# Performance work log

Hardware: AMD Instinct MI355X
Metric: run time of the kernel (lower is better)

The kernel has to match this reference:

```python
import jax, jax.numpy as jnp
import numpy as np

K = 16      # neighbors per node (hard-coded in ParticleNet)
EPS = 1e-5  # BatchNorm eps


def _forward(x, convs, fcW1, fcb1, fcW2, fcb2):
    # x: [B, N, F0]; convs: list of 3 layer-lists of (W, b, gamma, beta)
    B, N, _ = x.shape
    for c, layers in enumerate(convs):
        feat = x[..., :2] if c == 0 else x            # first kNN uses coords only
        sq = jnp.sum(feat * feat, axis=-1)            # [B, N]
        d2 = sq[:, :, None] + sq[:, None, :] - 2.0 * jnp.einsum('bnf,bmf->bnm', feat, feat)
        d2 = d2 + jnp.eye(N, dtype=d2.dtype) * 1e9    # exclude self-loops (knn_graph loop=False)
        idx = jax.lax.top_k(-d2, K)[1]                # [B, N, K] nearest-neighbor indices
        x_j = jax.vmap(lambda xb, ib: xb[ib])(x, idx) # gather neighbors -> [B, N, K, F]
        x_i = jnp.broadcast_to(x[:, :, None, :], x_j.shape)
        h = jnp.concatenate([x_i, x_j - x_i], axis=-1)  # PyG EdgeConv message input
        for (W, b, g, e) in layers:                   # Linear -> BatchNorm1d(train) -> ReLU
            h = h @ W + b
            m = h.mean(axis=(0, 1, 2))
            v = h.var(axis=(0, 1, 2))
            h = jax.nn.relu(g * (h - m) * jax.lax.rsqrt(v + EPS) + e)
        x = jnp.concatenate([h.mean(axis=2), x], axis=-1)  # aggr='mean', then skip-concat
    pooled = x.mean(axis=1)                           # global_mean_pool -> [B, 451]
    return (pooled @ fcW1 + fcb1) @ fcW2 + fcb2       # fc1 (no act) then fc2


def setup_inputs() -> dict:
    key = jax.random.key(0)
    B, N, F = 128, 128, 3
    ins, outs = [6, 134, 390], [64, 128, 256]
    d = {}
    ki = [0]
    def nk():
        ki[0] += 1
        return jax.random.fold_in(key, ki[0])
    d['x'] = jax.random.normal(nk(), (B, N, F), jnp.float32)
    for c in range(3):
        dims = [(ins[c], outs[c]), (outs[c], outs[c]), (outs[c], outs[c])]
        for l, (fi, fo) in enumerate(dims):
            d[f'W{c}{l}'] = jax.random.normal(nk(), (fi, fo), jnp.float32) / np.sqrt(fi).astype(np.float32)
            d[f'b{c}{l}'] = jnp.zeros((fo,), jnp.float32)
            d[f'g{c}{l}'] = jnp.ones((fo,), jnp.float32)
            d[f'e{c}{l}'] = jnp.zeros((fo,), jnp.float32)
    d['fcW1'] = jax.random.normal(nk(), (451, 256), jnp.float32) / np.float32(np.sqrt(451))
    d['fcb1'] = jnp.zeros((256,), jnp.float32)
    d['fcW2'] = jax.random.normal(nk(), (256, 5), jnp.float32) / np.float32(np.sqrt(256))
    d['fcb2'] = jnp.zeros((5,), jnp.float32)
    return d


def reference(x,
              W00, b00, g00, e00, W01, b01, g01, e01, W02, b02, g02, e02,
              W10, b10, g10, e10, W11, b11, g11, e11, W12, b12, g12, e12,
              W20, b20, g20, e20, W21, b21, g21, e21, W22, b22, g22, e22,
              fcW1, fcb1, fcW2, fcb2):
    convs = [
        [(W00, b00, g00, e00), (W01, b01, g01, e01), (W02, b02, g02, e02)],
        [(W10, b10, g10, e10), (W11, b11, g11, e11), (W12, b12, g12, e12)],
        [(W20, b20, g20, e20), (W21, b21, g21, e21), (W22, b22, g22, e22)],
    ]
    return _forward(x, convs, fcW1, fcb1, fcW2, fcb2)
```

## Files before the change

kernel.cpp:

```cpp
#include <hip/hip_runtime.h>
#include <hip/hip_bf16.h>
#include <type_traits>

typedef __hip_bfloat16 bf16;
typedef short v8s __attribute__((ext_vector_type(8)));
typedef short v2s __attribute__((ext_vector_type(2)));
typedef float v4f __attribute__((ext_vector_type(4)));

__device__ __forceinline__ float b2f(bf16 v) { return __bfloat162float(v); }
__device__ __forceinline__ bf16  f2b(float v) { return __float2bfloat16(v); }
__device__ __forceinline__ short f2bs(float v) {
    bf16 b = f2b(v); short s; __builtin_memcpy(&s, &b, 2); return s;
}
__device__ __forceinline__ float bs2f(short s) {
    bf16 b; __builtin_memcpy(&b, &s, 2); return b2f(b);
}

#define NB 128
#define NN 128
#define KNN 16
#define M_NODES (NB * NN)
#define NPOS ((long)M_NODES * KNN)
#define NREP 16

__device__ __forceinline__ void fold_stats(const float* __restrict__ st, int c,
                                           float& sum, float& sq) {
    sum = 0.f; sq = 0.f;
#pragma unroll
    for (int r = 0; r < NREP; ++r) { sum += st[r * 512 + c]; sq += st[r * 512 + 256 + c]; }
}

__device__ __forceinline__ int swz_tile(int bid) {
    int xcd = bid & 7;
    int slot = bid >> 3;
    int batch = xcd * 16 + (slot >> 5);
    int tile = slot & 31;
    return batch * 32 + tile;
}

__global__ void zero_kernel(float* __restrict__ p, int n) {
    int i = blockIdx.x * blockDim.x + threadIdx.x;
    if (i < n) p[i] = 0.f;
}

__global__ __launch_bounds__(256) void wconv_kernel(const float* __restrict__ W,
        short* __restrict__ Wt, int O) {
    int d = blockIdx.x * 256 + threadIdx.x;
    int c = d / O, k = d - c * O;
    Wt[d] = f2bs(W[(size_t)k * O + c]);
}

__global__ __launch_bounds__(256) void wconv0_kernel(const float* __restrict__ W,
        short* __restrict__ Wd, short* __restrict__ Wb, int F, int Fpad, int O) {
    int d = blockIdx.x * 256 + threadIdx.x;
    if (d >= O * Fpad) return;
    int c = d / Fpad, k = d - c * Fpad;
    if (k < F) {
        float wt = W[(size_t)k * O + c];
        float wb = W[(size_t)(F + k) * O + c];
        Wd[d] = f2bs(wt - wb);
        Wb[d] = f2bs(wb);
    } else { Wd[d] = 0; Wb[d] = 0; }
}

__global__ __launch_bounds__(256) void sq_kernel(const float* __restrict__ x, int C, int D,
                                                 float* __restrict__ sq) {
    int n = blockIdx.x * 256 + threadIdx.x;
    if (n >= M_NODES) return;
    float s = 0.f;
    for (int d = 0; d < D; ++d) { float v = x[(size_t)n * C + d]; s += v * v; }
    sq[n] = s;
}

__global__ __launch_bounds__(256) void dist_kernel(const float* __restrict__ x, int C, int D,
                                                   const float* __restrict__ sq,
                                                   float* __restrict__ d2) {
    __shared__ float As[16][65];
    __shared__ float Bs[16][65];
    const int tid = threadIdx.x;
    const int tx = tid & 15, ty = tid >> 4;
    const int m0 = blockIdx.y * 64;
    const int b  = m0 >> 7;
    const int c0 = blockIdx.x * 64;
    float acc[4][4];
#pragma unroll
    for (int r = 0; r < 4; ++r)
#pragma unroll
        for (int c = 0; c < 4; ++c) acc[r][c] = 0.f;
    for (int k0 = 0; k0 < D; k0 += 16) {
        for (int l = tid; l < 1024; l += 256) {
            int k = l & 15, m = l >> 4;
            int kk = k0 + k;
            As[k][m] = (kk < D) ? x[(size_t)(m0 + m) * C + kk] : 0.f;
            Bs[k][m] = (kk < D) ? x[(size_t)(b * NN + c0 + m) * C + kk] : 0.f;
        }
        __syncthreads();
        for (int k = 0; k < 16; ++k) {
            float av[4], bv[4];
#pragma unroll
            for (int r = 0; r < 4; ++r) av[r] = As[k][ty + 16 * r];
#pragma unroll
            for (int c = 0; c < 4; ++c) bv[c] = Bs[k][tx + 16 * c];
#pragma unroll
            for (int r = 0; r < 4; ++r)
#pragma unroll
                for (int c = 0; c < 4; ++c) acc[r][c] += av[r] * bv[c];
        }
        __syncthreads();
    }
#pragma unroll
    for (int r = 0; r < 4; ++r)
#pragma unroll
        for (int c = 0; c < 4; ++c) {
            int m = m0 + ty + 16 * r;
            int jl = c0 + tx + 16 * c;
            int jg = b * NN + jl;
            float v = sq[m] + sq[jg] - 2.0f * acc[r][c];
            if (m == jg) v += 1e9f;
            d2[(size_t)m * NN + jl] = v;
        }
}

__global__ __launch_bounds__(256) void knn_select_kernel(const float* __restrict__ d2,
                                                         int* __restrict__ idx) {
    const int node = blockIdx.x * 4 + (threadIdx.x >> 6);
    const int lane = threadIdx.x & 63;
    const float* row = d2 + (size_t)node * NN;
    float v0 = row[lane], v1 = row[lane + 64];
    int j0 = lane, j1 = lane + 64;
    int myIdx = 0;
#pragma unroll
    for (int k = 0; k < KNN; ++k) {
        float bv; int bj;
        if (v1 < v0 || (v1 == v0 && j1 < j0)) { bv = v1; bj = j1; }
        else                                 { bv = v0; bj = j0; }
#pragma unroll
        for (int off = 32; off; off >>= 1) {
            float ov = __shfl_xor(bv, off);
            int oj = __shfl_xor(bj, off);
            if (ov < bv || (ov == bv && oj < bj)) { bv = ov; bj = oj; }
        }
        if (bj == j0) v0 = 3.0e38f;
        if (bj == j1) v1 = 3.0e38f;
        if (lane == k) myIdx = bj;
    }
    if (lane < KNN) idx[(size_t)node * KNN + lane] = myIdx;
}

template<int O>
__global__ __launch_bounds__(256, 2) void node_gemm_mfma(
    const float* __restrict__ x, int F, int Fpad,
    const short* __restrict__ Wd, const short* __restrict__ Wb,
    const float* __restrict__ bias,
    float* __restrict__ T1, float* __restrict__ T2)
{
    constexpr int CPW = O / 64;
    __shared__ __align__(16) short Am[64][232];
    const int tid = threadIdx.x;
    const int lane = tid & 63, wave = tid >> 6;
    const int l15 = lane & 15, quad = lane >> 4;
    const int m0 = blockIdx.x * 64;
    for (int l = tid; l < 64 * Fpad; l += 256) {
        int m = l / Fpad, k = l - m * Fpad;
        Am[m][k] = (k < F) ? f2bs(x[(size_t)(m0 + m) * F + k]) : (short)0;
    }
    __syncthreads();
#pragma unroll
    for (int p = 0; p < 2; ++p) {
        const short* __restrict__ Wg = p ? Wb : Wd;
        float* __restrict__ T = p ? T2 : T1;
        v4f acc[4][CPW];
#pragma unroll
        for (int rt = 0; rt < 4; ++rt)
#pragma unroll
            for (int j = 0; j < CPW; ++j)
#pragma unroll
                for (int r = 0; r < 4; ++r) acc[rt][j][r] = 0.f;
        for (int k0 = 0; k0 < Fpad; k0 += 32) {
            v8s av[4];
#pragma unroll
            for (int rt = 0; rt < 4; ++rt)
                av[rt] = *(const v8s*)&Am[rt * 16 + l15][k0 + quad * 8];
#pragma unroll
            for (int j = 0; j < CPW; ++j) {
                int c = (wave * CPW + j) * 16 + l15;
                v8s bv = *(const v8s*)&Wg[(size_t)c * Fpad + k0 + quad * 8];
#pragma unroll
                for (int rt = 0; rt < 4; ++rt)
                    acc[rt][j] = __builtin_amdgcn_mfma_f32_16x16x32_bf16(av[rt], bv, acc[rt][j], 0, 0, 0);
            }
        }
#pragma unroll
        for (int j = 0; j < CPW; ++j) {
            int c = (wave * CPW + j) * 16 + l15;
            float bb = p ? 0.f : bias[c];
#pragma unroll
            for (int rt = 0; rt < 4; ++rt)
#pragma unroll
                for (int r = 0; r < 4; ++r)
                    T[(size_t)(m0 + rt * 16 + quad * 4 + r) * O + c] = acc[rt][j][r] + bb;
        }
    }
}

template<int O>
__global__ __launch_bounds__(256) void stats0_lds_kernel(
    const float* __restrict__ T1, const float* __restrict__ T2,
    const int* __restrict__ idx, float* __restrict__ st0)
{
    constexpr int CH = (O > 128) ? 128 : O;
    constexpr int NG = 256 / CH;
    constexpr int NPG = NN / NG;
    __shared__ float T2s[NN][CH];
    __shared__ int idxs[NN * KNN];
    __shared__ float redS[NG][CH], redQ[NG][CH];
    const int tid = threadIdx.x;
    const int nchunk = O / CH;
    const int b = blockIdx.x / nchunk;
    const int c0 = (blockIdx.x - b * nchunk) * CH;
    const int rep = blockIdx.x & (NREP - 1);

    for (int l = tid; l < NN * CH; l += 256) {
        int n = l / CH, c = l - n * CH;
        T2s[n][c] = T2[(size_t)(b * NN + n) * O + c0 + c];
    }
    for (int l = tid; l < NN * KNN; l += 256) idxs[l] = idx[(size_t)b * NN * KNN + l];
    __syncthreads();

    const int c = tid & (CH - 1);
    const int g = tid / CH;
    float s = 0.f, q = 0.f;
    for (int n = g * NPG; n < (g + 1) * NPG; ++n) {
        float t1 = T1[(size_t)(b * NN + n) * O + c0 + c];
#pragma unroll
        for (int k = 0; k < KNN; ++k) {
            int j = idxs[n * KNN + k];
            float v = t1 + T2s[j][c];
            s += v; q += v * v;
        }
    }
    redS[g][c] = s; redQ[g][c] = q;
    __syncthreads();
    if (g == 0) {
#pragma unroll
        for (int gg = 1; gg < NG; ++gg) { s += redS[gg][c]; q += redQ[gg][c]; }
        atomicAdd(&st0[rep * 512 + c0 + c], s);
        atomicAdd(&st0[rep * 512 + 256 + c0 + c], q);
    }
}


template<int O>
__global__ __launch_bounds__(256, 4) void gemm1_kernel(
    const float* __restrict__ T1, const float* __restrict__ T2, const int* __restrict__ idx,
    const short* __restrict__ W1, const float* __restrict__ bias1,
    const float* __restrict__ gm0, const float* __restrict__ bt0,
    const float* __restrict__ st0, float* __restrict__ st1,
    short* __restrict__ h, float inv_n)
{
    constexpr int CPW = O / 64;
    constexpr int OSH = (O == 64) ? 6 : (O == 128 ? 7 : 8);
    constexpr int AP = O + 8;
    __shared__ __align__(16) short Am[64][AP];
    __shared__ float T1s[4 * O];
    __shared__ float sc0[O], sh0[O];
    __shared__ int gArr[64];
    const int tid = threadIdx.x;
    const int lane = tid & 63, wave = tid >> 6;
    const int l15 = lane & 15, quad = lane >> 4;
    const int work = swz_tile(blockIdx.x);
    const int e0 = work * 64;
    const int nb0 = e0 >> 4;
    const int rep = work & (NREP - 1);

    if (tid < 64) {
        int e = e0 + tid;
        int nd = e >> 4;
        gArr[tid] = ((nd >> 7) << 7) + idx[e];
    }
    for (int l = tid; l < 4 * O; l += 256)
        T1s[l] = T1[(size_t)(nb0 + (l >> OSH)) * O + (l & (O - 1))];
    if (tid < O) {
        float sum, sq;
        fold_stats(st0, tid, sum, sq);
        float mean = sum * inv_n;
        float var = fmaxf(sq * inv_n - mean * mean, 0.f);
        float s = rsqrtf(var + 1e-5f) * gm0[tid];
        sc0[tid] = s; sh0[tid] = bt0[tid] - mean * s;
    }
    __syncthreads();

    for (int l = tid; l < 32 * O; l += 256) {
        int m = l >> (OSH - 1);
        int c = (l & (O / 2 - 1)) * 2;
        const float2 t2 = *(const float2*)&T2[(size_t)gArr[m] * O + c];
        const int tb = (m >> 4) * O + c;
        float v0 = fmaxf((T1s[tb] + t2.x) * sc0[c] + sh0[c], 0.f);
        float v1 = fmaxf((T1s[tb + 1] + t2.y) * sc0[c + 1] + sh0[c + 1], 0.f);
        v2s pr; pr[0] = f2bs(v0); pr[1] = f2bs(v1);
        *(v2s*)&Am[m][c] = pr;
    }
    __syncthreads();

    v4f acc[4][CPW];
#pragma unroll
    for (int rt = 0; rt < 4; ++rt)
#pragma unroll
        for (int j = 0; j < CPW; ++j)
#pragma unroll
            for (int r = 0; r < 4; ++r) acc[rt][j][r] = 0.f;

    v8s bvc[CPW];
#pragma unroll
    for (int j = 0; j < CPW; ++j) {
        int c = (wave * CPW + j) * 16 + l15;
        bvc[j] = *(const v8s*)&W1[(size_t)c * O + quad * 8];
    }
#pragma unroll
    for (int k0 = 0; k0 < O; k0 += 32) {
        v8s bvn[CPW];
        if (k0 + 32 < O) {
#pragma unroll
            for (int j = 0; j < CPW; ++j) {
                int c = (wave * CPW + j) * 16 + l15;
                bvn[j] = *(const v8s*)&W1[(size_t)c * O + k0 + 32 + quad * 8];
            }
        }
        v8s av[4];
#pragma unroll
        for (int rt = 0; rt < 4; ++rt)
            av[rt] = *(const v8s*)&Am[rt * 16 + l15][k0 + quad * 8];
#pragma unroll
        for (int j = 0; j < CPW; ++j)
#pragma unroll
            for (int rt = 0; rt < 4; ++rt)
                acc[rt][j] = __builtin_amdgcn_mfma_f32_16x16x32_bf16(av[rt], bvc[j], acc[rt][j], 0, 0, 0);
        if (k0 + 32 < O) {
#pragma unroll
            for (int j = 0; j < CPW; ++j) bvc[j] = bvn[j];
        }
    }
#pragma unroll
    for (int j = 0; j < CPW; ++j) {
        float bb = bias1[(wave * CPW + j) * 16 + l15];
#pragma unroll
        for (int rt = 0; rt < 4; ++rt)
#pragma unroll
            for (int r = 0; r < 4; ++r) acc[rt][j][r] += bb;
    }
#pragma unroll
    for (int j = 0; j < CPW; ++j) {
        int c = (wave * CPW + j) * 16 + l15;
        float s = 0.f, q = 0.f;
#pragma unroll
        for (int rt = 0; rt < 4; ++rt)
#pragma unroll
            for (int r = 0; r < 4; ++r) { float v = acc[rt][j][r]; s += v; q += v * v; }
        s += __shfl_down(s, 32); s += __shfl_down(s, 16);
        q += __shfl_down(q, 32); q += __shfl_down(q, 16);
        if (quad == 0) { atomicAdd(&st1[rep * 512 + c], s); atomicAdd(&st1[rep * 512 + 256 + c], q); }
    }
    __syncthreads();
#pragma unroll
    for (int j = 0; j < CPW; ++j) {
        int c = (wave * CPW + j) * 16 + l15;
#pragma unroll
        for (int rt = 0; rt < 4; ++rt)
#pragma unroll
            for (int r = 0; r < 4; ++r)
                Am[rt * 16 + quad * 4 + r][c] = f2bs(acc[rt][j][r]);
    }
    __syncthreads();
    for (int g = tid; g < 8 * O; g += 256) {
        int row = g >> (OSH - 3);
        int c8 = (g & (O / 8 - 1)) * 8;
        *(v8s*)&h[(size_t)(e0 + row) * O + c8] = *(const v8s*)&Am[row][c8];
    }
}

template<int O>
__global__ __launch_bounds__(256, 4) void gemm2_kernel(
    short* __restrict__ h,
    const short* __restrict__ W2, const float* __restrict__ bias2,
    const float* __restrict__ gm1, const float* __restrict__ bt1,
    const float* __restrict__ st1, float* __restrict__ st2, float inv_n)
{
    constexpr int CPW = O / 64;
    constexpr int OSH = (O == 64) ? 6 : (O == 128 ? 7 : 8);
    constexpr int AP = O + 8;
    __shared__ __align__(16) short Am[64][AP];
    __shared__ float sc1[O], sh1[O];
    const int tid = threadIdx.x;
    const int lane = tid & 63, wave = tid >> 6;
    const int l15 = lane & 15, quad = lane >> 4;
    const int work = swz_tile(blockIdx.x);
    const int e0 = work * 64;
    const int rep = work & (NREP - 1);

    if (tid < O) {
        float sum, sq;
        fold_stats(st1, tid, sum, sq);
        float mean = sum * inv_n;
        float var = fmaxf(sq * inv_n - mean * mean, 0.f);
        float s = rsqrtf(var + 1e-5f) * gm1[tid];
        sc1[tid] = s; sh1[tid] = bt1[tid] - mean * s;
    }
    __syncthreads();

    for (int g = tid; g < 8 * O; g += 256) {
        int row = g >> (OSH - 3);
        int c8 = (g & (O / 8 - 1)) * 8;
        v8s hv = *(const v8s*)&h[(size_t)(e0 + row) * O + c8];
        v8s ov;
#pragma unroll
        for (int j = 0; j < 8; ++j) {
            float v = bs2f(hv[j]) * sc1[c8 + j] + sh1[c8 + j];
            ov[j] = f2bs(fmaxf(v, 0.f));
        }
        *(v8s*)&Am[row][c8] = ov;
    }
    __syncthreads();

    v4f acc[4][CPW];
#pragma unroll
    for (int rt = 0; rt < 4; ++rt)
#pragma unroll
        for (int j = 0; j < CPW; ++j)
#pragma unroll
            for (int r = 0; r < 4; ++r) acc[rt][j][r] = 0.f;

    v8s bvc[CPW];
#pragma unroll
    for (int j = 0; j < CPW; ++j) {
        int c = (wave * CPW + j) * 16 + l15;
        bvc[j] = *(const v8s*)&W2[(size_t)c * O + quad * 8];
    }
#pragma unroll
    for (int k0 = 0; k0 < O; k0 += 32) {
        v8s bvn[CPW];
        if (k0 + 32 < O) {
#pragma unroll
            for (int j = 0; j < CPW; ++j) {
                int c = (wave * CPW + j) * 16 + l15;
                bvn[j] = *(const v8s*)&W2[(size_t)c * O + k0 + 32 + quad * 8];
            }
        }
        v8s av[4];
#pragma unroll
        for (int rt = 0; rt < 4; ++rt)
            av[rt] = *(const v8s*)&Am[rt * 16 + l15][k0 + quad * 8];
#pragma unroll
        for (int j = 0; j < CPW; ++j)
#pragma unroll
            for (int rt = 0; rt < 4; ++rt)
                acc[rt][j] = __builtin_amdgcn_mfma_f32_16x16x32_bf16(av[rt], bvc[j], acc[rt][j], 0, 0, 0);
        if (k0 + 32 < O) {
#pragma unroll
            for (int j = 0; j < CPW; ++j) bvc[j] = bvn[j];
        }
    }
#pragma unroll
    for (int j = 0; j < CPW; ++j) {
        float bb = bias2[(wave * CPW + j) * 16 + l15];
#pragma unroll
        for (int rt = 0; rt < 4; ++rt)
#pragma unroll
            for (int r = 0; r < 4; ++r) acc[rt][j][r] += bb;
    }
#pragma unroll
    for (int j = 0; j < CPW; ++j) {
        int c = (wave * CPW + j) * 16 + l15;
        float s = 0.f, q = 0.f;
#pragma unroll
        for (int rt = 0; rt < 4; ++rt)
#pragma unroll
            for (int r = 0; r < 4; ++r) { float v = acc[rt][j][r]; s += v; q += v * v; }
        s += __shfl_down(s, 32); s += __shfl_down(s, 16);
        q += __shfl_down(q, 32); q += __shfl_down(q, 16);
        if (quad == 0) { atomicAdd(&st2[rep * 512 + c], s); atomicAdd(&st2[rep * 512 + 256 + c], q); }
    }
    __syncthreads();
#pragma unroll
    for (int j = 0; j < CPW; ++j) {
        int c = (wave * CPW + j) * 16 + l15;
#pragma unroll
        for (int rt = 0; rt < 4; ++rt)
#pragma unroll
            for (int r = 0; r < 4; ++r)
                Am[rt * 16 + quad * 4 + r][c] = f2bs(acc[rt][j][r]);
    }
    __syncthreads();
    for (int g = tid; g < 8 * O; g += 256) {
        int row = g >> (OSH - 3);
        int c8 = (g & (O / 8 - 1)) * 8;
        *(v8s*)&h[(size_t)(e0 + row) * O + c8] = *(const v8s*)&Am[row][c8];
    }
}

template<int O>
__global__ __launch_bounds__(256) void finish_kernel(
    const short* __restrict__ h,
    const float* __restrict__ st2, const float* __restrict__ gm2, const float* __restrict__ bt2,
    const float* __restrict__ xold, float* __restrict__ xnew, int F, float inv_n)
{
    constexpr int G = 256 / O;
    constexpr int RPG = 64 / G;
    constexpr int NPG = RPG / 16;
    const int tid = threadIdx.x;
    const int c = tid & (O - 1);
    const int rg = tid / O;
    const int work = swz_tile(blockIdx.x);
    const int e0 = work * 64;
    const int nb0 = e0 >> 4;
    float sum, sq;
    fold_stats(st2, c, sum, sq);
    float mean = sum * inv_n;
    float var = fmaxf(sq * inv_n - mean * mean, 0.f);
    float sc = rsqrtf(var + 1e-5f) * gm2[c];
    float sh = bt2[c] - mean * sc;
    float s[NPG];
#pragma unroll
    for (int i = 0; i < NPG; ++i) s[i] = 0.f;
    const int m0 = rg * RPG;
#pragma unroll
    for (int r = 0; r < RPG; ++r) {
        float v = bs2f(h[(size_t)(e0 + m0 + r) * O + c]) * sc + sh;
        s[r >> 4] += fmaxf(v, 0.f);
    }
    const int Cnew = O + F;
#pragma unroll
    for (int i = 0; i < NPG; ++i)
        xnew[(size_t)(nb0 + rg * NPG + i) * Cnew + c] = s[i] * (1.0f / 16.0f);
    for (int l = tid; l < 4 * F; l += 256) {
        int nd = l / F, cc = l - nd * F;
        xnew[(size_t)(nb0 + nd) * Cnew + O + cc] = xold[(size_t)(nb0 + nd) * F + cc];
    }
}

__global__ __launch_bounds__(256) void pool_kernel(const float* __restrict__ x, float* __restrict__ pooled, int C) {
    int b = blockIdx.x, t = threadIdx.x;
    for (int c = t; c < C; c += 256) {
        float s = 0.f;
        for (int n = 0; n < NN; ++n) s += x[(size_t)(b * NN + n) * C + c];
        pooled[b * C + c] = s * (1.0f / NN);
    }
}

__global__ __launch_bounds__(256) void fc_kernel(const float* __restrict__ pooled,
                                                 const float* __restrict__ W1, const float* __restrict__ b1,
                                                 const float* __restrict__ W2, const float* __restrict__ b2,
                                                 float* __restrict__ out, int C) {
    __shared__ float px[451];
    __shared__ float h1[256];
    int b = blockIdx.x, t = threadIdx.x;
    for (int c = t; c < C; c += 256) px[c] = pooled[b * C + c];
    __syncthreads();
    float s = 0.f;
    for (int i = 0; i < C; ++i) s += px[i] * W1[(size_t)i * 256 + t];
    h1[t] = s + b1[t];
    __syncthreads();
    if (t < 5) {
        float s2 = 0.f;
        for (int j = 0; j < 256; ++j) s2 += h1[j] * W2[j * 5 + t];
        out[b * 5 + t] = s2 + b2[t];
    }
}

extern "C" void kernel_launch(void* const* d_in, const int* in_sizes, int n_in,
                              void* d_out, int out_size, void* d_ws, size_t ws_size,
                              hipStream_t stream) {
    const float* xin = (const float*)d_in[0];
    auto Wp = [&](int c, int l) { return (const float*)d_in[1 + c * 12 + l * 4 + 0]; };
    auto Bp = [&](int c, int l) { return (const float*)d_in[1 + c * 12 + l * 4 + 1]; };
    auto Gp = [&](int c, int l) { return (const float*)d_in[1 + c * 12 + l * 4 + 2]; };
    auto Ep = [&](int c, int l) { return (const float*)d_in[1 + c * 12 + l * 4 + 3]; };
    const float* fcW1 = (const float*)d_in[37];
    const float* fcb1 = (const float*)d_in[38];
    const float* fcW2 = (const float*)d_in[39];
    const float* fcb2 = (const float*)d_in[40];

    char* ws = (char*)d_ws;
    size_t off = 0;
    auto alloc = [&](size_t bytes) -> void* {
        void* p = ws + off;
        off += (bytes + 255) & ~(size_t)255;
        return p;
    };
    const int M = M_NODES;
    float* x1     = (float*)alloc((size_t)M * 67 * 4);
    float* x2     = (float*)alloc((size_t)M * 195 * 4);
    float* x3     = (float*)alloc((size_t)M * 451 * 4);
    float* T1     = (float*)alloc((size_t)M * 256 * 4);
    float* T2     = (float*)alloc((size_t)M * 256 * 4);
    int*   idxb   = (int*)alloc((size_t)M * KNN * 4);
    float* stats  = (float*)alloc((size_t)3 * NREP * 512 * 4);
    float* pooled = (float*)alloc((size_t)NB * 451 * 4);
    short* W1b    = (short*)alloc(256 * 256 * 2);
    short* W2b    = (short*)alloc(256 * 256 * 2);
    short* W0d    = (short*)alloc(256 * 224 * 2);
    short* W0b    = (short*)alloc(256 * 224 * 2);
    float* d2buf  = (float*)alloc((size_t)M * NN * 4);
    float* sqbuf  = (float*)alloc((size_t)M * 4);
    short* hbuf   = (short*)alloc((size_t)NPOS * 256 * 2);
    (void)in_sizes; (void)n_in; (void)out_size; (void)ws_size;

    float* st0 = stats;
    float* st1 = stats + NREP * 512;
    float* st2 = stats + 2 * NREP * 512;
    const float inv_n = 1.0f / (float)NPOS;

    auto run_conv = [&](const float* xc, float* xn, int F, int D, int O, int c) {
        const int Fpad = (F + 31) & ~31;
        sq_kernel<<<M / 256, 256, 0, stream>>>(xc, F, D, sqbuf);
        dist_kernel<<<dim3(2, M / 64), 256, 0, stream>>>(xc, F, D, sqbuf, d2buf);
        knn_select_kernel<<<M / 4, 256, 0, stream>>>(d2buf, idxb);
        wconv0_kernel<<<(O * Fpad + 255) / 256, 256, 0, stream>>>(Wp(c, 0), W0d, W0b, F, Fpad, O);
        wconv_kernel<<<O * O / 256, 256, 0, stream>>>(Wp(c, 1), W1b, O);
        wconv_kernel<<<O * O / 256, 256, 0, stream>>>(Wp(c, 2), W2b, O);
        zero_kernel<<<3 * NREP * 2, 256, 0, stream>>>(stats, 3 * NREP * 512);
        const int grid = (int)(NPOS / 64);
        auto launch = [&](auto tag) {
            constexpr int OO = decltype(tag)::value;
            node_gemm_mfma<OO><<<M / 64, 256, 0, stream>>>(xc, F, Fpad, W0d, W0b, Bp(c, 0), T1, T2);
            stats0_lds_kernel<OO><<<NB * (OO > 128 ? 2 : 1), 256, 0, stream>>>(T1, T2, idxb, st0);
            gemm1_kernel<OO><<<grid, 256, 0, stream>>>(T1, T2, idxb, W1b, Bp(c, 1),
                Gp(c, 0), Ep(c, 0), st0, st1, hbuf, inv_n);
            gemm2_kernel<OO><<<grid, 256, 0, stream>>>(hbuf, W2b, Bp(c, 2),
                Gp(c, 1), Ep(c, 1), st1, st2, inv_n);
            finish_kernel<OO><<<grid, 256, 0, stream>>>(hbuf, st2, Gp(c, 2), Ep(c, 2),
                xc, xn, F, inv_n);
        };
        if (O == 64)       launch(std::integral_constant<int, 64>{});
        else if (O == 128) launch(std::integral_constant<int, 128>{});
        else               launch(std::integral_constant<int, 256>{});
    };

    run_conv(xin, x1, 3, 2, 64, 0);
    run_conv(x1, x2, 67, 67, 128, 1);
    run_conv(x2, x3, 195, 195, 256, 2);
    pool_kernel<<<NB, 256, 0, stream>>>(x3, pooled, 451);
    fc_kernel<<<NB, 256, 0, stream>>>(pooled, fcW1, fcb1, fcW2, fcb2, (float*)d_out, 451);
}
```

Before: 990.6 us.

## Scale edge-tile rows with channel width, fuse prep kernels, compute norms in-distance

Makes the rows per block of the gemm1/gemm2/finish kernels depend on the output width (256 for O=64, 128 for O=128, 64 for O=256), with the tile swizzle parameterised to match. This gives narrower layers more MFMA work per block and fewer blocks. Zeroing the stats and the three weight conversions are merged into one prep kernel, and the separate squared-norm kernel is folded into the distance kernel, which cuts several launches per conv. The A-operand loads in the MFMA loops are also reordered to keep fewer fragments live, and gemm1 now reads T1 from global memory instead of staging it in LDS, at the cost of more LDS and registers per block for the small-O cases.

```diff
diff --git a/kernel.cpp b/kernel.cpp
--- a/kernel.cpp
+++ b/kernel.cpp
@@ -30,50 +30,51 @@
     for (int r = 0; r < NREP; ++r) { sum += st[r * 512 + c]; sq += st[r * 512 + 256 + c]; }
 }
 
+template<int TPB>
 __device__ __forceinline__ int swz_tile(int bid) {
     int xcd = bid & 7;
     int slot = bid >> 3;
-    int batch = xcd * 16 + (slot >> 5);
-    int tile = slot & 31;
-    return batch * 32 + tile;
-}
-
-__global__ void zero_kernel(float* __restrict__ p, int n) {
-    int i = blockIdx.x * blockDim.x + threadIdx.x;
-    if (i < n) p[i] = 0.f;
-}
-
-__global__ __launch_bounds__(256) void wconv_kernel(const float* __restrict__ W,
-        short* __restrict__ Wt, int O) {
-    int d = blockIdx.x * 256 + threadIdx.x;
-    int c = d / O, k = d - c * O;
-    Wt[d] = f2bs(W[(size_t)k * O + c]);
-}
-
-__global__ __launch_bounds__(256) void wconv0_kernel(const float* __restrict__ W,
-        short* __restrict__ Wd, short* __restrict__ Wb, int F, int Fpad, int O) {
-    int d = blockIdx.x * 256 + threadIdx.x;
-    if (d >= O * Fpad) return;
-    int c = d / Fpad, k = d - c * Fpad;
-    if (k < F) {
-        float wt = W[(size_t)k * O + c];
-        float wb = W[(size_t)(F + k) * O + c];
-        Wd[d] = f2bs(wt - wb);
-        Wb[d] = f2bs(wb);
-    } else { Wd[d] = 0; Wb[d] = 0; }
-}
-
-__global__ __launch_bounds__(256) void sq_kernel(const float* __restrict__ x, int C, int D,
-                                                 float* __restrict__ sq) {
-    int n = blockIdx.x * 256 + threadIdx.x;
-    if (n >= M_NODES) return;
-    float s = 0.f;
-    for (int d = 0; d < D; ++d) { float v = x[(size_t)n * C + d]; s += v * v; }
-    sq[n] = s;
+    int batch = xcd * 16 + slot / TPB;
+    int tile = slot - (slot / TPB) * TPB;
+    return batch * TPB + tile;
+}
+
+__global__ __launch_bounds__(256) void prep_kernel(
+    const float* __restrict__ W0, const float* __restrict__ W1, const float* __restrict__ W2,
+    short* __restrict__ W0d, short* __restrict__ W0b,
+    short* __restrict__ W1b, short* __restrict__ W2b,
+    float* __restrict__ stats, int F, int Fpad, int O)
+{
+    int i = blockIdx.x * 256 + threadIdx.x;
+    const int nz = 3 * NREP * 512;
+    if (i < nz) { stats[i] = 0.f; return; }
+    i -= nz;
+    const int n0 = O * Fpad;
+    if (i < n0) {
+        int c = i / Fpad, k = i - c * Fpad;
+        if (k < F) {
+            float wt = W0[(size_t)k * O + c];
+            float wb = W0[(size_t)(F + k) * O + c];
+            W0d[i] = f2bs(wt - wb);
+            W0b[i] = f2bs(wb);
+        } else { W0d[i] = 0; W0b[i] = 0; }
+        return;
+    }
+    i -= n0;
+    const int n1 = O * O;
+    if (i < n1) {
+        int c = i / O, k = i - c * O;
+        W1b[i] = f2bs(W1[(size_t)k * O + c]);
+        return;
+    }
+    i -= n1;
+    if (i < n1) {
+        int c = i / O, k = i - c * O;
+        W2b[i] = f2bs(W2[(size_t)k * O + c]);
+    }
 }
 
 __global__ __launch_bounds__(256) void dist_kernel(const float* __restrict__ x, int C, int D,
-                                                   const float* __restrict__ sq,
                                                    float* __restrict__ d2) {
     __shared__ float As[16][65];
     __shared__ float Bs[16][65];
@@ -82,11 +83,11 @@
     const int m0 = blockIdx.y * 64;
     const int b  = m0 >> 7;
     const int c0 = blockIdx.x * 64;
-    float acc[4][4];
-#pragma unroll
-    for (int r = 0; r < 4; ++r)
-#pragma unroll
-        for (int c = 0; c < 4; ++c) acc[r][c] = 0.f;
+    float acc[4][4], rn[4], cn[4];
+#pragma unroll
+    for (int r = 0; r < 4; ++r) { rn[r] = 0.f; cn[r] = 0.f;
+#pragma unroll
+        for (int c = 0; c < 4; ++c) acc[r][c] = 0.f; }
     for (int k0 = 0; k0 < D; k0 += 16) {
         for (int l = tid; l < 1024; l += 256) {
             int k = l & 15, m = l >> 4;
@@ -98,9 +99,9 @@
         for (int k = 0; k < 16; ++k) {
             float av[4], bv[4];
 #pragma unroll
-            for (int r = 0; r < 4; ++r) av[r] = As[k][ty + 16 * r];
-#pragma unroll
-            for (int c = 0; c < 4; ++c) bv[c] = Bs[k][tx + 16 * c];
+            for (int r = 0; r < 4; ++r) { av[r] = As[k][ty + 16 * r]; rn[r] += av[r] * av[r]; }
+#pragma unroll
+            for (int c = 0; c < 4; ++c) { bv[c] = Bs[k][tx + 16 * c]; cn[c] += bv[c] * bv[c]; }
 #pragma unroll
             for (int r = 0; r < 4; ++r)
 #pragma unroll
@@ -115,7 +116,7 @@
             int m = m0 + ty + 16 * r;
             int jl = c0 + tx + 16 * c;
             int jg = b * NN + jl;
-            float v = sq[m] + sq[jg] - 2.0f * acc[r][c];
+            float v = rn[r] + cn[c] - 2.0f * acc[r][c];
             if (m == jg) v += 1e9f;
             d2[(size_t)m * NN + jl] = v;
         }
@@ -177,17 +178,15 @@
 #pragma unroll
                 for (int r = 0; r < 4; ++r) acc[rt][j][r] = 0.f;
         for (int k0 = 0; k0 < Fpad; k0 += 32) {
-            v8s av[4];
-#pragma unroll
-            for (int rt = 0; rt < 4; ++rt)
-                av[rt] = *(const v8s*)&Am[rt * 16 + l15][k0 + quad * 8];
-#pragma unroll
-            for (int j = 0; j < CPW; ++j) {
-                int c = (wave * CPW + j) * 16 + l15;
-                v8s bv = *(const v8s*)&Wg[(size_t)c * Fpad + k0 + quad * 8];
-#pragma unroll
-                for (int rt = 0; rt < 4; ++rt)
-                    acc[rt][j] = __builtin_amdgcn_mfma_f32_16x16x32_bf16(av[rt], bv, acc[rt][j], 0, 0, 0);
+#pragma unroll
+            for (int rt = 0; rt < 4; ++rt) {
+                v8s av = *(const v8s*)&Am[rt * 16 + l15][k0 + quad * 8];
+#pragma unroll
+                for (int j = 0; j < CPW; ++j) {
+                    int c = (wave * CPW + j) * 16 + l15;
+                    v8s bv = *(const v8s*)&Wg[(size_t)c * Fpad + k0 + quad * 8];
+                    acc[rt][j] = __builtin_amdgcn_mfma_f32_16x16x32_bf16(av, bv, acc[rt][j], 0, 0, 0);
+                }
             }
         }
 #pragma unroll
@@ -250,7 +249,7 @@
 }
 
 
-template<int O>
+template<int O, int ROWS>
 __global__ __launch_bounds__(256, 4) void gemm1_kernel(
     const float* __restrict__ T1, const float* __restrict__ T2, const int* __restrict__ idx,
     const short* __restrict__ W1, const float* __restrict__ bias1,
@@ -259,27 +258,26 @@
     short* __restrict__ h, float inv_n)
 {
     constexpr int CPW = O / 64;
+    constexpr int RT = ROWS / 16;
     constexpr int OSH = (O == 64) ? 6 : (O == 128 ? 7 : 8);
     constexpr int AP = O + 8;
-    __shared__ __align__(16) short Am[64][AP];
-    __shared__ float T1s[4 * O];
+    constexpr int TPB = 2048 / ROWS;
+    __shared__ __align__(16) short Am[ROWS][AP];
     __shared__ float sc0[O], sh0[O];
-    __shared__ int gArr[64];
+    __shared__ int gArr[ROWS];
     const int tid = threadIdx.x;
     const int lane = tid & 63, wave = tid >> 6;
     const int l15 = lane & 15, quad = lane >> 4;
-    const int work = swz_tile(blockIdx.x);
-    const int e0 = work * 64;
+    const int work = swz_tile<TPB>(blockIdx.x);
+    const int e0 = work * ROWS;
     const int nb0 = e0 >> 4;
     const int rep = work & (NREP - 1);
 
-    if (tid < 64) {
-        int e = e0 + tid;
+    for (int l = tid; l < ROWS; l += 256) {
+        int e = e0 + l;
         int nd = e >> 4;
-        gArr[tid] = ((nd >> 7) << 7) + idx[e];
-    }
-    for (int l = tid; l < 4 * O; l += 256)
-        T1s[l] = T1[(size_t)(nb0 + (l >> OSH)) * O + (l & (O - 1))];
+        gArr[l] = ((nd >> 7) << 7) + idx[e];
+    }
     if (tid < O) {
         float sum, sq;
         fold_stats(st0, tid, sum, sq);
@@ -290,21 +288,21 @@
     }
     __syncthreads();
 
-    for (int l = tid; l < 32 * O; l += 256) {
+    for (int l = tid; l < ROWS * O / 2; l += 256) {
         int m = l >> (OSH - 1);
         int c = (l & (O / 2 - 1)) * 2;
+        const float2 t1 = *(const float2*)&T1[(size_t)(nb0 + (m >> 4)) * O + c];
         const float2 t2 = *(const float2*)&T2[(size_t)gArr[m] * O + c];
-        const int tb = (m >> 4) * O + c;
-        float v0 = fmaxf((T1s[tb] + t2.x) * sc0[c] + sh0[c], 0.f);
-        float v1 = fmaxf((T1s[tb + 1] + t2.y) * sc0[c + 1] + sh0[c + 1], 0.f);
+        float v0 = fmaxf((t1.x + t2.x) * sc0[c] + sh0[c], 0.f);
+        float v1 = fmaxf((t1.y + t2.y) * sc0[c + 1] + sh0[c + 1], 0.f);
         v2s pr; pr[0] = f2bs(v0); pr[1] = f2bs(v1);
         *(v2s*)&Am[m][c] = pr;
     }
     __syncthreads();
 
-    v4f acc[4][CPW];
-#pragma unroll
-    for (int rt = 0; rt < 4; ++rt)
+    v4f acc[RT][CPW];
+#pragma unroll
+    for (int rt = 0; rt < RT; ++rt)
 #pragma unroll
         for (int j = 0; j < CPW; ++j)
 #pragma unroll
@@ -326,15 +324,13 @@
                 bvn[j] = *(const v8s*)&W1[(size_t)c * O + k0 + 32 + quad * 8];
             }
         }
-        v8s av[4];
-#pragma unroll
-        for (int rt = 0; rt < 4; ++rt)
-            av[rt] = *(const v8s*)&Am[rt * 16 + l15][k0 + quad * 8];
-#pragma unroll
-        for (int j = 0; j < CPW; ++j)
-#pragma unroll
-            for (int rt = 0; rt < 4; ++rt)
-                acc[rt][j] = __builtin_amdgcn_mfma_f32_16x16x32_bf16(av[rt], bvc[j], acc[rt][j], 0, 0, 0);
+#pragma unroll
+        for (int rt = 0; rt < RT; ++rt) {
+            v8s av = *(const v8s*)&Am[rt * 16 + l15][k0 + quad * 8];
+#pragma unroll
+            for (int j = 0; j < CPW; ++j)
+                acc[rt][j] = __builtin_amdgcn_mfma_f32_16x16x32_bf16(av, bvc[j], acc[rt][j], 0, 0, 0);
+        }
         if (k0 + 32 < O) {
 #pragma unroll
             for (int j = 0; j < CPW; ++j) bvc[j] = bvn[j];
@@ -344,7 +340,7 @@
     for (int j = 0; j < CPW; ++j) {
         float bb = bias1[(wave * CPW + j) * 16 + l15];
 #pragma unroll
-        for (int rt = 0; rt < 4; ++rt)
+        for (int rt = 0; rt < RT; ++rt)
 #pragma unroll
             for (int r = 0; r < 4; ++r) acc[rt][j][r] += bb;
     }
@@ -353,7 +349,7 @@
         int c = (wave * CPW + j) * 16 + l15;
         float s = 0.f, q = 0.f;
 #pragma unroll
-        for (int rt = 0; rt < 4; ++rt)
+        for (int rt = 0; rt < RT; ++rt)
 #pragma unroll
             for (int r = 0; r < 4; ++r) { float v = acc[rt][j][r]; s += v; q += v * v; }
         s += __shfl_down(s, 32); s += __shfl_down(s, 16);
@@ -365,20 +361,20 @@
     for (int j = 0; j < CPW; ++j) {
         int c = (wave * CPW + j) * 16 + l15;
 #pragma unroll
-        for (int rt = 0; rt < 4; ++rt)
+        for (int rt = 0; rt < RT; ++rt)
 #pragma unroll
             for (int r = 0; r < 4; ++r)
                 Am[rt * 16 + quad * 4 + r][c] = f2bs(acc[rt][j][r]);
     }
     __syncthreads();
-    for (int g = tid; g < 8 * O; g += 256) {
+    for (int g = tid; g < ROWS * O / 8; g += 256) {
         int row = g >> (OSH - 3);
         int c8 = (g & (O / 8 - 1)) * 8;
         *(v8s*)&h[(size_t)(e0 + row) * O + c8] = *(const v8s*)&Am[row][c8];
     }
 }
 
-template<int O>
+template<int O, int ROWS>
 __global__ __launch_bounds__(256, 4) void gemm2_kernel(
     short* __restrict__ h,
     const short* __restrict__ W2, const float* __restrict__ bias2,
@@ -386,15 +382,17 @@
     const float* __restrict__ st1, float* __restrict__ st2, float inv_n)
 {
     constexpr int CPW = O / 64;
+    constexpr int RT = ROWS / 16;
     constexpr int OSH = (O == 64) ? 6 : (O == 128 ? 7 : 8);
     constexpr int AP = O + 8;
-    __shared__ __align__(16) short Am[64][AP];
+    constexpr int TPB = 2048 / ROWS;
+    __shared__ __align__(16) short Am[ROWS][AP];
     __shared__ float sc1[O], sh1[O];
     const int tid = threadIdx.x;
     const int lane = tid & 63, wave = tid >> 6;
     const int l15 = lane & 15, quad = lane >> 4;
-    const int work = swz_tile(blockIdx.x);
-    const int e0 = work * 64;
+    const int work = swz_tile<TPB>(blockIdx.x);
+    const int e0 = work * ROWS;
     const int rep = work & (NREP - 1);
 
     if (tid < O) {
@@ -407,7 +405,7 @@
     }
     __syncthreads();
 
-    for (int g = tid; g < 8 * O; g += 256) {
+    for (int g = tid; g < ROWS * O / 8; g += 256) {
         int row = g >> (OSH - 3);
         int c8 = (g & (O / 8 - 1)) * 8;
         v8s hv = *(const v8s*)&h[(size_t)(e0 + row) * O + c8];
@@ -421,9 +419,9 @@
     }
     __syncthreads();
 
-    v4f acc[4][CPW];
-#pragma unroll
-    for (int rt = 0; rt < 4; ++rt)
+    v4f acc[RT][CPW];
+#pragma unroll
+    for (int rt = 0; rt < RT; ++rt)
 #pragma unroll
         for (int j = 0; j < CPW; ++j)
 #pragma unroll
@@ -445,15 +443,13 @@
                 bvn[j] = *(const v8s*)&W2[(size_t)c * O + k0 + 32 + quad * 8];
             }
         }
-        v8s av[4];
-#pragma unroll
-        for (int rt = 0; rt < 4; ++rt)
-            av[rt] = *(const v8s*)&Am[rt * 16 + l15][k0 + quad * 8];
-#pragma unroll
-        for (int j = 0; j < CPW; ++j)
-#pragma unroll
-            for (int rt = 0; rt < 4; ++rt)
-                acc[rt][j] = __builtin_amdgcn_mfma_f32_16x16x32_bf16(av[rt], bvc[j], acc[rt][j], 0, 0, 0);
+#pragma unroll
+        for (int rt = 0; rt < RT; ++rt) {
+            v8s av = *(const v8s*)&Am[rt * 16 + l15][k0 + quad * 8];
+#pragma unroll
+            for (int j = 0; j < CPW; ++j)
+                acc[rt][j] = __builtin_amdgcn_mfma_f32_16x16x32_bf16(av, bvc[j], acc[rt][j], 0, 0, 0);
+        }
         if (k0 + 32 < O) {
 #pragma unroll
             for (int j = 0; j < CPW; ++j) bvc[j] = bvn[j];
@@ -463,7 +459,7 @@
     for (int j = 0; j < CPW; ++j) {
         float bb = bias2[(wave * CPW + j) * 16 + l15];
 #pragma unroll
-        for (int rt = 0; rt < 4; ++rt)
+        for (int rt = 0; rt < RT; ++rt)
 #pragma unroll
             for (int r = 0; r < 4; ++r) acc[rt][j][r] += bb;
     }
@@ -472,7 +468,7 @@
         int c = (wave * CPW + j) * 16 + l15;
         float s = 0.f, q = 0.f;
 #pragma unroll
-        for (int rt = 0; rt < 4; ++rt)
+        for (int rt = 0; rt < RT; ++rt)
 #pragma unroll
             for (int r = 0; r < 4; ++r) { float v = acc[rt][j][r]; s += v; q += v * v; }
         s += __shfl_down(s, 32); s += __shfl_down(s, 16);
@@ -484,33 +480,35 @@
     for (int j = 0; j < CPW; ++j) {
         int c = (wave * CPW + j) * 16 + l15;
 #pragma unroll
-        for (int rt = 0; rt < 4; ++rt)
+        for (int rt = 0; rt < RT; ++rt)
 #pragma unroll
             for (int r = 0; r < 4; ++r)
                 Am[rt * 16 + quad * 4 + r][c] = f2bs(acc[rt][j][r]);
     }
     __syncthreads();
-    for (int g = tid; g < 8 * O; g += 256) {
+    for (int g = tid; g < ROWS * O / 8; g += 256) {
         int row = g >> (OSH - 3);
         int c8 = (g & (O / 8 - 1)) * 8;
         *(v8s*)&h[(size_t)(e0 + row) * O + c8] = *(const v8s*)&Am[row][c8];
     }
 }
 
-template<int O>
+template<int O, int ROWS>
 __global__ __launch_bounds__(256) void finish_kernel(
     const short* __restrict__ h,
     const float* __restrict__ st2, const float* __restrict__ gm2, const float* __restrict__ bt2,
     const float* __restrict__ xold, float* __restrict__ xnew, int F, float inv_n)
 {
     constexpr int G = 256 / O;
-    constexpr int RPG = 64 / G;
+    constexpr int RPG = ROWS / G;
     constexpr int NPG = RPG / 16;
+    constexpr int NPB = ROWS / 16;
+    constexpr int TPB = 2048 / ROWS;
     const int tid = threadIdx.x;
     const int c = tid & (O - 1);
     const int rg = tid / O;
-    const int work = swz_tile(blockIdx.x);
-    const int e0 = work * 64;
+    const int work = swz_tile<TPB>(blockIdx.x);
+    const int e0 = work * ROWS;
     const int nb0 = e0 >> 4;
     float sum, sq;
     fold_stats(st2, c, sum, sq);
@@ -531,7 +529,7 @@
 #pragma unroll
     for (int i = 0; i < NPG; ++i)
         xnew[(size_t)(nb0 + rg * NPG + i) * Cnew + c] = s[i] * (1.0f / 16.0f);
-    for (int l = tid; l < 4 * F; l += 256) {
+    for (int l = tid; l < NPB * F; l += 256) {
         int nd = l / F, cc = l - nd * F;
         xnew[(size_t)(nb0 + nd) * Cnew + O + cc] = xold[(size_t)(nb0 + nd) * F + cc];
     }
@@ -600,7 +598,6 @@
     short* W0d    = (short*)alloc(256 * 224 * 2);
     short* W0b    = (short*)alloc(256 * 224 * 2);
     float* d2buf  = (float*)alloc((size_t)M * NN * 4);
-    float* sqbuf  = (float*)alloc((size_t)M * 4);
     short* hbuf   = (short*)alloc((size_t)NPOS * 256 * 2);
     (void)in_sizes; (void)n_in; (void)out_size; (void)ws_size;
 
@@ -611,23 +608,22 @@
 
     auto run_conv = [&](const float* xc, float* xn, int F, int D, int O, int c) {
         const int Fpad = (F + 31) & ~31;
-        sq_kernel<<<M / 256, 256, 0, stream>>>(xc, F, D, sqbuf);
-        dist_kernel<<<dim3(2, M / 64), 256, 0, stream>>>(xc, F, D, sqbuf, d2buf);
+        dist_kernel<<<dim3(2, M / 64), 256, 0, stream>>>(xc, F, D, d2buf);
         knn_select_kernel<<<M / 4, 256, 0, stream>>>(d2buf, idxb);
-        wconv0_kernel<<<(O * Fpad + 255) / 256, 256, 0, stream>>>(Wp(c, 0), W0d, W0b, F, Fpad, O);
-        wconv_kernel<<<O * O / 256, 256, 0, stream>>>(Wp(c, 1), W1b, O);
-        wconv_kernel<<<O * O / 256, 256, 0, stream>>>(Wp(c, 2), W2b, O);
-        zero_kernel<<<3 * NREP * 2, 256, 0, stream>>>(stats, 3 * NREP * 512);
-        const int grid = (int)(NPOS / 64);
+        const int prepN = 3 * NREP * 512 + O * Fpad + 2 * O * O;
+        prep_kernel<<<(prepN + 255) / 256, 256, 0, stream>>>(Wp(c, 0), Wp(c, 1), Wp(c, 2),
+            W0d, W0b, W1b, W2b, stats, F, Fpad, O);
         auto launch = [&](auto tag) {
             constexpr int OO = decltype(tag)::value;
+            constexpr int RR = 16384 / OO;
+            const int grid = (int)(NPOS / RR);
             node_gemm_mfma<OO><<<M / 64, 256, 0, stream>>>(xc, F, Fpad, W0d, W0b, Bp(c, 0), T1, T2);
             stats0_lds_kernel<OO><<<NB * (OO > 128 ? 2 : 1), 256, 0, stream>>>(T1, T2, idxb, st0);
-            gemm1_kernel<OO><<<grid, 256, 0, stream>>>(T1, T2, idxb, W1b, Bp(c, 1),
+            gemm1_kernel<OO, RR><<<grid, 256, 0, stream>>>(T1, T2, idxb, W1b, Bp(c, 1),
                 Gp(c, 0), Ep(c, 0), st0, st1, hbuf, inv_n);
-            gemm2_kernel<OO><<<grid, 256, 0, stream>>>(hbuf, W2b, Bp(c, 2),
+            gemm2_kernel<OO, RR><<<grid, 256, 0, stream>>>(hbuf, W2b, Bp(c, 2),
                 Gp(c, 1), Ep(c, 1), st1, st2, inv_n);
-            finish_kernel<OO><<<grid, 256, 0, stream>>>(hbuf, st2, Gp(c, 2), Ep(c, 2),
+            finish_kernel<OO, RR><<<grid, 256, 0, stream>>>(hbuf, st2, Gp(c, 2), Ep(c, 2),
                 xc, xn, F, inv_n);
         };
         if (O == 64)       launch(std::integral_constant<int, 64>{});
```

New measurement: 870.9 us. 1.14x faster.
